# Kernel tuning notes

Hardware: AMD Instinct MI355X
Metric: run time of the kernel (lower is better)

The kernel has to match this reference:

```python
import jax, jax.numpy as jnp
import numpy as np

N = 50000
IN_F = 200
OUT_F = 200
NRELA = 200
E1 = 400000
E2 = 100000
ALPHA = 0.2  # leakyrelu slope


def setup_inputs() -> dict:
    key = jax.random.key(0)
    ks = jax.random.split(key, 9)
    xav = float(np.sqrt(2.0 / (OUT_F + 2 * IN_F + NRELA))) * 1.414
    return {
        "x": jax.random.normal(ks[0], (N, IN_F), dtype=jnp.float32),
        "edge": jax.random.randint(ks[1], (2, E1), 0, N, dtype=jnp.int32),
        "edge_embed": jax.random.normal(ks[2], (E1, NRELA), dtype=jnp.float32),
        "edge_list_nhop": jax.random.randint(ks[3], (2, E2), 0, N, dtype=jnp.int32),
        "edge_embed_nhop": jax.random.normal(ks[4], (E2, NRELA), dtype=jnp.float32),
        "a": jax.random.normal(ks[5], (OUT_F, 2 * IN_F + NRELA), dtype=jnp.float32) * xav,
        "a_2": jax.random.normal(ks[6], (1, OUT_F), dtype=jnp.float32) * float(np.sqrt(2.0 / (1 + OUT_F))) * 1.414,
        "mlp_w": jax.random.normal(ks[7], (1, OUT_F), dtype=jnp.float32) * float(np.sqrt(1.0 / OUT_F)),
        "mlp_b": jnp.zeros((1,), dtype=jnp.float32),
    }


def reference(x, edge, edge_embed, edge_list_nhop, edge_embed_nhop, a, a_2, mlp_w, mlp_b):
    # concat 1-hop and n-hop edges: e [2,E], emb [E,nrela]
    e = jnp.concatenate([edge, edge_list_nhop], axis=1)
    emb = jnp.concatenate([edge_embed, edge_embed_nhop], axis=0)
    src = e[0]
    dst = e[1]
    n_edges = emb.shape[0]
    # edge_h: [E, 2*in + nrela]
    edge_h = jnp.concatenate([x[src], x[dst], emb], axis=1)
    # edge_m = a @ edge_h.T, kept as [E, out]
    edge_m = edge_h @ a.T
    # powers = -leakyrelu(a_2 @ edge_m): [E]
    powers = -jax.nn.leaky_relu(edge_m @ a_2[0], ALPHA)
    # inline MLP: tanh(Linear(edge_m)) -> [E]
    y = jnp.tanh(edge_m @ mlp_w[0] + mlp_b[0])
    powers = powers * y / n_edges
    edge_e = jnp.exp(powers)  # [E]
    n = x.shape[0]
    # segment-sum over source nodes (sparse.sum over dim=1 of coo[src,dst,:])
    e_rowsum = jax.ops.segment_sum(edge_e, src, num_segments=n)[:, None]  # [N,1]
    e_rowsum = jnp.where(e_rowsum == 0.0, 1e-12, e_rowsum)
    # weighted scatter-add of edge messages
    edge_w = edge_e[:, None] * edge_m  # [E, out]
    h_prime = jax.ops.segment_sum(edge_w, src, num_segments=n)  # [N, out]
    h_prime = h_prime / e_rowsum
    return jax.nn.elu(h_prime)  # concat=True
```

## Files before the change

kernel.cpp:

```cpp
#include <hip/hip_runtime.h>
#include <math.h>

#define NN    50000
#define FDIM  200
#define E1N   400000
#define E2N   100000
#define EN    500000

typedef __attribute__((ext_vector_type(8))) short short8;
typedef __attribute__((ext_vector_type(4))) float f32x4;

#define VALL_OFF   0
#define WALL_OFF   608
#define SCAL_OFF   1216
#define RS_OFF     201216
#define CNT_OFF    251216
#define FILL_OFF   301216
#define INCL_OFF   351216
#define BSUM_OFF   401216
#define SORT_OFF   401472
#define XB_OFF     1401472
#define AB_OFF     6401472
#define TSB_OFF    6461472

static __device__ __forceinline__ unsigned short f2bf(float f) {
    unsigned int u = __float_as_uint(f);
    unsigned int r = (u + 0x7fffu + ((u >> 16) & 1u)) >> 16;
    return (unsigned short)r;
}
static __device__ __forceinline__ float bf2f(unsigned short s) {
    return __uint_as_float((unsigned int)s << 16);
}

__global__ void k_coeffs(const float* __restrict__ a, const float* __restrict__ a2,
                         const float* __restrict__ mlpw,
                         float* __restrict__ vall, float* __restrict__ wall) {
    int k = blockIdx.x * blockDim.x + threadIdx.x;
    if (k >= 600) return;
    float v = 0.f, w = 0.f;
    for (int o = 0; o < FDIM; ++o) {
        float av = a[o * 600 + k];
        v += a2[o] * av;
        w += mlpw[o] * av;
    }
    vall[k] = v;
    wall[k] = w;
}

__global__ __launch_bounds__(256) void k_node_scal(const float* __restrict__ x,
                                                   const float* __restrict__ vall,
                                                   const float* __restrict__ wall,
                                                   float* __restrict__ scal,
                                                   unsigned short* __restrict__ xb) {
    __shared__ float sv[1200];
    int tid = threadIdx.x;
    for (int i = tid; i < 1200; i += 256) sv[i] = (i < 600) ? vall[i] : wall[i - 600];
    __syncthreads();
    int lane = tid & 63;
    int n = blockIdx.x * 4 + (tid >> 6);
    float ps = 0.f, pd = 0.f, qs = 0.f, qd = 0.f;
    if (lane < 50) {
        float4 xv = *(const float4*)(x + (size_t)n * FDIM + lane * 4);
        float4 v1 = *(const float4*)(sv + lane * 4);
        float4 v2 = *(const float4*)(sv + 200 + lane * 4);
        float4 w1 = *(const float4*)(sv + 600 + lane * 4);
        float4 w2 = *(const float4*)(sv + 800 + lane * 4);
        ps = xv.x * v1.x + xv.y * v1.y + xv.z * v1.z + xv.w * v1.w;
        pd = xv.x * v2.x + xv.y * v2.y + xv.z * v2.z + xv.w * v2.w;
        qs = xv.x * w1.x + xv.y * w1.y + xv.z * w1.z + xv.w * w1.w;
        qd = xv.x * w2.x + xv.y * w2.y + xv.z * w2.z + xv.w * w2.w;
        ushort4 o;
        o.x = f2bf(xv.x); o.y = f2bf(xv.y); o.z = f2bf(xv.z); o.w = f2bf(xv.w);
        *(ushort4*)(xb + (size_t)n * FDIM + lane * 4) = o;
    }
    #pragma unroll
    for (int off = 32; off > 0; off >>= 1) {
        ps += __shfl_xor(ps, off);
        pd += __shfl_xor(pd, off);
        qs += __shfl_xor(qs, off);
        qd += __shfl_xor(qd, off);
    }
    if (lane == 0) {
        float4 r = make_float4(ps, pd, qs, qd);
        *(float4*)(scal + (size_t)n * 4) = r;
    }
}

__global__ __launch_bounds__(256) void k_cvt(const float* __restrict__ src,
                                             unsigned short* __restrict__ dst, int n4) {
    int i = blockIdx.x * 256 + threadIdx.x;
    if (i >= n4) return;
    float4 v = *(const float4*)(src + (size_t)i * 4);
    ushort4 o;
    o.x = f2bf(v.x); o.y = f2bf(v.y); o.z = f2bf(v.z); o.w = f2bf(v.w);
    *(ushort4*)(dst + (size_t)i * 4) = o;
}

__global__ __launch_bounds__(256) void k_hist(const int* __restrict__ edge,
                                              const int* __restrict__ edgenh,
                                              int* __restrict__ counts) {
    int g = blockIdx.x * 256 + threadIdx.x;
    if (g >= EN) return;
    int s = (g < E1N) ? edge[g] : edgenh[g - E1N];
    atomicAdd(counts + s, 1);
}

__global__ __launch_bounds__(256) void k_scan1(const int* __restrict__ counts,
                                               int* __restrict__ incl,
                                               int* __restrict__ bsums) {
    __shared__ int tmp[256];
    int g = blockIdx.x * 256 + threadIdx.x;
    int v = (g < NN) ? counts[g] : 0;
    tmp[threadIdx.x] = v;
    __syncthreads();
    for (int off = 1; off < 256; off <<= 1) {
        int t = (threadIdx.x >= off) ? tmp[threadIdx.x - off] : 0;
        __syncthreads();
        tmp[threadIdx.x] += t;
        __syncthreads();
    }
    if (g < NN) incl[g] = tmp[threadIdx.x];
    if (threadIdx.x == 255) bsums[blockIdx.x] = tmp[255];
}

__global__ __launch_bounds__(256) void k_scan2(int* __restrict__ bsums, int nb) {
    __shared__ int tmp[256];
    int v = (threadIdx.x < nb) ? bsums[threadIdx.x] : 0;
    tmp[threadIdx.x] = v;
    __syncthreads();
    for (int off = 1; off < 256; off <<= 1) {
        int t = (threadIdx.x >= off) ? tmp[threadIdx.x - off] : 0;
        __syncthreads();
        tmp[threadIdx.x] += t;
        __syncthreads();
    }
    if (threadIdx.x < nb) bsums[threadIdx.x] = tmp[threadIdx.x] - v;
}

__global__ __launch_bounds__(256) void k_scan3(const int* __restrict__ counts,
                                               int* __restrict__ incl,
                                               const int* __restrict__ bsums,
                                               int* __restrict__ fill) {
    int g = blockIdx.x * 256 + threadIdx.x;
    if (g >= NN) return;
    int v = incl[g] - counts[g] + bsums[blockIdx.x];
    incl[g] = v;
    fill[g] = v;
}

__global__ __launch_bounds__(256) void k_scatter(const int* __restrict__ edge,
                                                 const int* __restrict__ edgenh,
                                                 int* __restrict__ fill,
                                                 int2* __restrict__ sorted2) {
    int g = blockIdx.x * 256 + threadIdx.x;
    if (g >= EN) return;
    int s, d;
    if (g < E1N) { s = edge[g]; d = edge[E1N + g]; }
    else { s = edgenh[g - E1N]; d = edgenh[E2N + (g - E1N)]; }
    int pos = atomicAdd(fill + s, 1);
    sorted2[pos] = make_int2(g, d);
}

__global__ __launch_bounds__(256) void k_csr(const int2* __restrict__ sorted2,
                                             const int* __restrict__ offs,
                                             const int* __restrict__ counts,
                                             const float* __restrict__ ee,
                                             const float* __restrict__ eenh,
                                             const unsigned short* __restrict__ xb,
                                             const float* __restrict__ vall,
                                             const float* __restrict__ wall,
                                             const float* __restrict__ scal,
                                             const float* __restrict__ mlpb,
                                             float* __restrict__ rowsum,
                                             unsigned short* __restrict__ Tsb) {
    int tid = threadIdx.x, lane = tid & 63;
    int n = blockIdx.x * 4 + (tid >> 6);
    float4 v3 = make_float4(0, 0, 0, 0), w3 = v3;
    if (lane < 50) {
        v3 = *(const float4*)(vall + 400 + lane * 4);
        w3 = *(const float4*)(wall + 400 + lane * 4);
    }
    float4 sc_n = *(const float4*)(scal + (size_t)n * 4);
    float mb = mlpb[0];
    int beg = offs[n], cnt = counts[n];
    float accx0 = 0, accx1 = 0, accx2 = 0, accx3 = 0;
    float acce0 = 0, acce1 = 0, acce2 = 0, acce3 = 0;
    float rs = 0.f;
    int2 ed = (cnt > 0) ? sorted2[beg] : make_int2(0, 0);
    for (int i = 0; i < cnt; ++i) {
        int2 ed_n = (i + 1 < cnt) ? sorted2[beg + i + 1] : ed;
        int e = ed.x, d = ed.y;
        const float* erow = (e < E1N) ? ee + (size_t)e * FDIM
                                      : eenh + (size_t)(e - E1N) * FDIM;
        float4 ev = make_float4(0, 0, 0, 0), xv = ev;
        if (lane < 50) {
            ev = *(const float4*)(erow + lane * 4);
            ushort4 xu = *(const ushort4*)(xb + (size_t)d * FDIM + lane * 4);
            xv.x = bf2f(xu.x); xv.y = bf2f(xu.y); xv.z = bf2f(xu.z); xv.w = bf2f(xu.w);
        }
        float pe = ev.x * v3.x + ev.y * v3.y + ev.z * v3.z + ev.w * v3.w;
        float qe = ev.x * w3.x + ev.y * w3.y + ev.z * w3.z + ev.w * w3.w;
        #pragma unroll
        for (int off = 32; off > 0; off >>= 1) {
            pe += __shfl_xor(pe, off);
            qe += __shfl_xor(qe, off);
        }
        float4 sd = *(const float4*)(scal + (size_t)d * 4);
        float z1 = sc_n.x + sd.y + pe;
        float z2 = sc_n.z + sd.w + qe + mb;
        float l = z1 > 0.f ? z1 : 0.2f * z1;
        float e2 = __expf(2.f * z2);
        float t = 1.f - 2.f * __builtin_amdgcn_rcpf(e2 + 1.f);
        float wgt = __expf(l * t * (-1.f / (float)EN));
        rs += wgt;
        accx0 += wgt * xv.x; accx1 += wgt * xv.y; accx2 += wgt * xv.z; accx3 += wgt * xv.w;
        acce0 += wgt * ev.x; acce1 += wgt * ev.y; acce2 += wgt * ev.z; acce3 += wgt * ev.w;
        ed = ed_n;
    }
    if (lane == 0) rowsum[n] = rs;
    float inv = (cnt > 0) ? __builtin_amdgcn_rcpf(rs) : 0.f;
    if (lane < 50) {
        ushort4 o1, o2;
        o1.x = f2bf(accx0 * inv); o1.y = f2bf(accx1 * inv);
        o1.z = f2bf(accx2 * inv); o1.w = f2bf(accx3 * inv);
        o2.x = f2bf(acce0 * inv); o2.y = f2bf(acce1 * inv);
        o2.z = f2bf(acce2 * inv); o2.w = f2bf(acce3 * inv);
        *(ushort4*)(Tsb + (size_t)n * 400 + lane * 4) = o1;
        *(ushort4*)(Tsb + (size_t)n * 400 + 200 + lane * 4) = o2;
    }
}

__global__ __launch_bounds__(256) void k_gemm_fused(const unsigned short* __restrict__ xb,
                                                    const unsigned short* __restrict__ tsb,
                                                    const unsigned short* __restrict__ ab,
                                                    const float* __restrict__ rowsum,
                                                    float* __restrict__ out) {
    __shared__ unsigned short Al[64][40];
    __shared__ unsigned short Bl[64][40];
    int tid = threadIdx.x, w = tid >> 6, lane = tid & 63;
    int bx = blockIdx.x, by = blockIdx.y;
    f32x4 acc[4] = {};
    int r = tid >> 2, c = tid & 3;
    int arow = by * 64 + r;
    int brow = bx * 64 + r;
    bool inA = arow < NN;
    bool inB = brow < 200;
    const unsigned short* aPx = xb + (size_t)arow * 200;
    const unsigned short* aPt = tsb + (size_t)arow * 400;
    const unsigned short* bP = ab + (size_t)brow * 600;
    for (int k0 = 0; k0 < 640; k0 += 32) {
        int gk = k0 + c * 8;
        uint4 av = make_uint4(0, 0, 0, 0), bv = av;
        if (gk < 200) {
            if (inA) av = *(const uint4*)(aPx + gk);
            if (inB) bv = *(const uint4*)(bP + gk);
        } else if (gk >= 224 && gk < 624) {
            if (inA) av = *(const uint4*)(aPt + (gk - 224));
            if (inB) bv = *(const uint4*)(bP + gk - 24);
        }
        *(uint4*)&Al[r][c * 8] = av;
        *(uint4*)&Bl[r][c * 8] = bv;
        __syncthreads();
        short8 af = *(short8*)&Al[w * 16 + (lane & 15)][(lane >> 4) * 8];
        #pragma unroll
        for (int ct = 0; ct < 4; ++ct) {
            short8 bf = *(short8*)&Bl[ct * 16 + (lane & 15)][(lane >> 4) * 8];
            acc[ct] = __builtin_amdgcn_mfma_f32_16x16x32_bf16(af, bf, acc[ct], 0, 0, 0);
        }
        __syncthreads();
    }
    #pragma unroll
    for (int ct = 0; ct < 4; ++ct) {
        #pragma unroll
        for (int rr = 0; rr < 4; ++rr) {
            int grow = by * 64 + w * 16 + (lane >> 4) * 4 + rr;
            int gcol = bx * 64 + ct * 16 + (lane & 15);
            if (grow < NN && gcol < 200) {
                float rsv = rowsum[grow];
                float h = acc[ct][rr];
                float o = (rsv == 0.f) ? 0.f : (h > 0.f ? h : expm1f(h));
                out[(size_t)grow * 200 + gcol] = o;
            }
        }
    }
}

extern "C" void kernel_launch(void* const* d_in, const int* in_sizes, int n_in,
                              void* d_out, int out_size, void* d_ws, size_t ws_size,
                              hipStream_t stream) {
    const float* x      = (const float*)d_in[0];
    const int*   edge   = (const int*)d_in[1];
    const float* ee     = (const float*)d_in[2];
    const int*   edgenh = (const int*)d_in[3];
    const float* eenh   = (const float*)d_in[4];
    const float* a      = (const float*)d_in[5];
    const float* a2     = (const float*)d_in[6];
    const float* mlpw   = (const float*)d_in[7];
    const float* mlpb   = (const float*)d_in[8];

    float* ws = (float*)d_ws;
    float* vall   = ws + VALL_OFF;
    float* wall   = ws + WALL_OFF;
    float* scal   = ws + SCAL_OFF;
    float* rowsum = ws + RS_OFF;
    int*   counts = (int*)(ws + CNT_OFF);
    int*   fill   = (int*)(ws + FILL_OFF);
    int*   incl   = (int*)(ws + INCL_OFF);
    int*   bsums  = (int*)(ws + BSUM_OFF);
    int2*  sorted2 = (int2*)(ws + SORT_OFF);
    unsigned short* xb  = (unsigned short*)(ws + XB_OFF);
    unsigned short* ab  = (unsigned short*)(ws + AB_OFF);
    unsigned short* tsb = (unsigned short*)(ws + TSB_OFF);

    hipMemsetAsync(counts, 0, (size_t)(2 * NN) * sizeof(int), stream);

    k_coeffs<<<3, 256, 0, stream>>>(a, a2, mlpw, vall, wall);
    k_node_scal<<<NN / 4, 256, 0, stream>>>(x, vall, wall, scal, xb);
    k_cvt<<<(200 * 600 / 4 + 255) / 256, 256, 0, stream>>>(a, ab, 200 * 600 / 4);

    k_hist<<<(EN + 255) / 256, 256, 0, stream>>>(edge, edgenh, counts);
    int nb = (NN + 255) / 256;
    k_scan1<<<nb, 256, 0, stream>>>(counts, incl, bsums);
    k_scan2<<<1, 256, 0, stream>>>(bsums, nb);
    k_scan3<<<nb, 256, 0, stream>>>(counts, incl, bsums, fill);
    k_scatter<<<(EN + 255) / 256, 256, 0, stream>>>(edge, edgenh, fill, sorted2);

    k_csr<<<NN / 4, 256, 0, stream>>>(sorted2, incl, counts, ee, eenh, xb,
                                      vall, wall, scal, mlpb, rowsum, tsb);

    dim3 gg(4, (NN + 63) / 64);
    k_gemm_fused<<<gg, 256, 0, stream>>>(xb, tsb, ab, rowsum, (float*)d_out);
}
```

Measured before the change: 747.2 us.

## Split edge weight computation into per-edge kernel and remap GEMM block order

Per-edge attention weights are now computed in a separate edge-parallel kernel that writes a weight buffer and accumulates row sums with atomics. The CSR aggregation kernel then only gathers edge embeddings and neighbour features scaled by the precomputed weight, which removes the serial shuffle-reduction and exp chain from its per-node loop. The GEMM block index is also remapped to a swizzled order to change cache locality. The cost is reading every edge embedding twice (once per kernel) plus an extra launch and atomics.

```diff
diff --git a/kernel.cpp b/kernel.cpp
--- a/kernel.cpp
+++ b/kernel.cpp
@@ -22,6 +22,7 @@
 #define XB_OFF     1401472
 #define AB_OFF     6401472
 #define TSB_OFF    6461472
+#define WGT_OFF    16461472
 
 static __device__ __forceinline__ unsigned short f2bf(float f) {
     unsigned int u = __float_as_uint(f);
@@ -161,70 +162,91 @@
     sorted2[pos] = make_int2(g, d);
 }
 
-__global__ __launch_bounds__(256) void k_csr(const int2* __restrict__ sorted2,
-                                             const int* __restrict__ offs,
-                                             const int* __restrict__ counts,
-                                             const float* __restrict__ ee,
-                                             const float* __restrict__ eenh,
-                                             const unsigned short* __restrict__ xb,
-                                             const float* __restrict__ vall,
-                                             const float* __restrict__ wall,
-                                             const float* __restrict__ scal,
-                                             const float* __restrict__ mlpb,
-                                             float* __restrict__ rowsum,
-                                             unsigned short* __restrict__ Tsb) {
+__global__ __launch_bounds__(256) void k_edge_wgt(const int* __restrict__ edge,
+                                                  const int* __restrict__ edgenh,
+                                                  const float* __restrict__ ee,
+                                                  const float* __restrict__ eenh,
+                                                  const float* __restrict__ vall,
+                                                  const float* __restrict__ wall,
+                                                  const float* __restrict__ scal,
+                                                  const float* __restrict__ mlpb,
+                                                  float* __restrict__ wgtbuf,
+                                                  float* __restrict__ rowsum) {
+    int tid = threadIdx.x, lane = tid & 63;
+    int e = blockIdx.x * 4 + (tid >> 6);
+    int s, d;
+    const float* erow;
+    if (e < E1N) {
+        s = edge[e]; d = edge[E1N + e];
+        erow = ee + (size_t)e * FDIM;
+    } else {
+        int f = e - E1N;
+        s = edgenh[f]; d = edgenh[E2N + f];
+        erow = eenh + (size_t)f * FDIM;
+    }
+    float pe = 0.f, qe = 0.f;
+    if (lane < 50) {
+        float4 ev = *(const float4*)(erow + lane * 4);
+        float4 v3 = *(const float4*)(vall + 400 + lane * 4);
+        float4 w3 = *(const float4*)(wall + 400 + lane * 4);
+        pe = ev.x * v3.x + ev.y * v3.y + ev.z * v3.z + ev.w * v3.w;
+        qe = ev.x * w3.x + ev.y * w3.y + ev.z * w3.z + ev.w * w3.w;
+    }
+    #pragma unroll
+    for (int off = 32; off > 0; off >>= 1) {
+        pe += __shfl_xor(pe, off);
+        qe += __shfl_xor(qe, off);
+    }
+    float4 ss = *(const float4*)(scal + (size_t)s * 4);
+    float4 sd = *(const float4*)(scal + (size_t)d * 4);
+    float z1 = ss.x + sd.y + pe;
+    float z2 = ss.z + sd.w + qe + mlpb[0];
+    float l = z1 > 0.f ? z1 : 0.2f * z1;
+    float e2 = __expf(2.f * z2);
+    float t = 1.f - 2.f * __builtin_amdgcn_rcpf(e2 + 1.f);
+    float w = __expf(l * t * (-1.f / (float)EN));
+    if (lane == 0) {
+        wgtbuf[e] = w;
+        atomicAdd(rowsum + s, w);
+    }
+}
+
+__global__ __launch_bounds__(256) void k_csr2(const int2* __restrict__ sorted2,
+                                              const int* __restrict__ offs,
+                                              const int* __restrict__ counts,
+                                              const float* __restrict__ ee,
+                                              const float* __restrict__ eenh,
+                                              const unsigned short* __restrict__ xb,
+                                              const float* __restrict__ wgtbuf,
+                                              const float* __restrict__ rowsum,
+                                              unsigned short* __restrict__ Tsb) {
     int tid = threadIdx.x, lane = tid & 63;
     int n = blockIdx.x * 4 + (tid >> 6);
-    float4 v3 = make_float4(0, 0, 0, 0), w3 = v3;
-    if (lane < 50) {
-        v3 = *(const float4*)(vall + 400 + lane * 4);
-        w3 = *(const float4*)(wall + 400 + lane * 4);
-    }
-    float4 sc_n = *(const float4*)(scal + (size_t)n * 4);
-    float mb = mlpb[0];
     int beg = offs[n], cnt = counts[n];
-    float accx0 = 0, accx1 = 0, accx2 = 0, accx3 = 0;
-    float acce0 = 0, acce1 = 0, acce2 = 0, acce3 = 0;
-    float rs = 0.f;
-    int2 ed = (cnt > 0) ? sorted2[beg] : make_int2(0, 0);
+    float ax0 = 0, ax1 = 0, ax2 = 0, ax3 = 0;
+    float ae0 = 0, ae1 = 0, ae2 = 0, ae3 = 0;
+    #pragma unroll 2
     for (int i = 0; i < cnt; ++i) {
-        int2 ed_n = (i + 1 < cnt) ? sorted2[beg + i + 1] : ed;
-        int e = ed.x, d = ed.y;
-        const float* erow = (e < E1N) ? ee + (size_t)e * FDIM
-                                      : eenh + (size_t)(e - E1N) * FDIM;
+        int2 ed = sorted2[beg + i];
+        float wv = wgtbuf[ed.x];
+        const float* erow = (ed.x < E1N) ? ee + (size_t)ed.x * FDIM
+                                         : eenh + (size_t)(ed.x - E1N) * FDIM;
         float4 ev = make_float4(0, 0, 0, 0), xv = ev;
         if (lane < 50) {
             ev = *(const float4*)(erow + lane * 4);
-            ushort4 xu = *(const ushort4*)(xb + (size_t)d * FDIM + lane * 4);
+            ushort4 xu = *(const ushort4*)(xb + (size_t)ed.y * FDIM + lane * 4);
             xv.x = bf2f(xu.x); xv.y = bf2f(xu.y); xv.z = bf2f(xu.z); xv.w = bf2f(xu.w);
         }
-        float pe = ev.x * v3.x + ev.y * v3.y + ev.z * v3.z + ev.w * v3.w;
-        float qe = ev.x * w3.x + ev.y * w3.y + ev.z * w3.z + ev.w * w3.w;
-        #pragma unroll
-        for (int off = 32; off > 0; off >>= 1) {
-            pe += __shfl_xor(pe, off);
-            qe += __shfl_xor(qe, off);
-        }
-        float4 sd = *(const float4*)(scal + (size_t)d * 4);
-        float z1 = sc_n.x + sd.y + pe;
-        float z2 = sc_n.z + sd.w + qe + mb;
-        float l = z1 > 0.f ? z1 : 0.2f * z1;
-        float e2 = __expf(2.f * z2);
-        float t = 1.f - 2.f * __builtin_amdgcn_rcpf(e2 + 1.f);
-        float wgt = __expf(l * t * (-1.f / (float)EN));
-        rs += wgt;
-        accx0 += wgt * xv.x; accx1 += wgt * xv.y; accx2 += wgt * xv.z; accx3 += wgt * xv.w;
-        acce0 += wgt * ev.x; acce1 += wgt * ev.y; acce2 += wgt * ev.z; acce3 += wgt * ev.w;
-        ed = ed_n;
-    }
-    if (lane == 0) rowsum[n] = rs;
-    float inv = (cnt > 0) ? __builtin_amdgcn_rcpf(rs) : 0.f;
+        ax0 += wv * xv.x; ax1 += wv * xv.y; ax2 += wv * xv.z; ax3 += wv * xv.w;
+        ae0 += wv * ev.x; ae1 += wv * ev.y; ae2 += wv * ev.z; ae3 += wv * ev.w;
+    }
+    float inv = (cnt > 0) ? __builtin_amdgcn_rcpf(rowsum[n]) : 0.f;
     if (lane < 50) {
         ushort4 o1, o2;
-        o1.x = f2bf(accx0 * inv); o1.y = f2bf(accx1 * inv);
-        o1.z = f2bf(accx2 * inv); o1.w = f2bf(accx3 * inv);
-        o2.x = f2bf(acce0 * inv); o2.y = f2bf(acce1 * inv);
-        o2.z = f2bf(acce2 * inv); o2.w = f2bf(acce3 * inv);
+        o1.x = f2bf(ax0 * inv); o1.y = f2bf(ax1 * inv);
+        o1.z = f2bf(ax2 * inv); o1.w = f2bf(ax3 * inv);
+        o2.x = f2bf(ae0 * inv); o2.y = f2bf(ae1 * inv);
+        o2.z = f2bf(ae2 * inv); o2.w = f2bf(ae3 * inv);
         *(ushort4*)(Tsb + (size_t)n * 400 + lane * 4) = o1;
         *(ushort4*)(Tsb + (size_t)n * 400 + 200 + lane * 4) = o2;
     }
@@ -238,7 +260,9 @@
     __shared__ unsigned short Al[64][40];
     __shared__ unsigned short Bl[64][40];
     int tid = threadIdx.x, w = tid >> 6, lane = tid & 63;
-    int bx = blockIdx.x, by = blockIdx.y;
+    int h = blockIdx.y * 4 + blockIdx.x;
+    int g = (h & 7) * 391 + (h >> 3);
+    int by = g >> 2, bx = g & 3;
     f32x4 acc[4] = {};
     int r = tid >> 2, c = tid & 3;
     int arow = by * 64 + r;
@@ -277,8 +301,8 @@
             int gcol = bx * 64 + ct * 16 + (lane & 15);
             if (grow < NN && gcol < 200) {
                 float rsv = rowsum[grow];
-                float h = acc[ct][rr];
-                float o = (rsv == 0.f) ? 0.f : (h > 0.f ? h : expm1f(h));
+                float hh = acc[ct][rr];
+                float o = (rsv == 0.f) ? 0.f : (hh > 0.f ? hh : expm1f(hh));
                 out[(size_t)grow * 200 + gcol] = o;
             }
         }
@@ -311,8 +335,9 @@
     unsigned short* xb  = (unsigned short*)(ws + XB_OFF);
     unsigned short* ab  = (unsigned short*)(ws + AB_OFF);
     unsigned short* tsb = (unsigned short*)(ws + TSB_OFF);
-
-    hipMemsetAsync(counts, 0, (size_t)(2 * NN) * sizeof(int), stream);
+    float* wgtbuf = ws + WGT_OFF;
+
+    hipMemsetAsync(rowsum, 0, (size_t)(3 * NN) * sizeof(int), stream);
 
     k_coeffs<<<3, 256, 0, stream>>>(a, a2, mlpw, vall, wall);
     k_node_scal<<<NN / 4, 256, 0, stream>>>(x, vall, wall, scal, xb);
@@ -325,8 +350,11 @@
     k_scan3<<<nb, 256, 0, stream>>>(counts, incl, bsums, fill);
     k_scatter<<<(EN + 255) / 256, 256, 0, stream>>>(edge, edgenh, fill, sorted2);
 
-    k_csr<<<NN / 4, 256, 0, stream>>>(sorted2, incl, counts, ee, eenh, xb,
-                                      vall, wall, scal, mlpb, rowsum, tsb);
+    k_edge_wgt<<<EN / 4, 256, 0, stream>>>(edge, edgenh, ee, eenh,
+                                           vall, wall, scal, mlpb, wgtbuf, rowsum);
+
+    k_csr2<<<NN / 4, 256, 0, stream>>>(sorted2, incl, counts, ee, eenh, xb,
+                                       wgtbuf, rowsum, tsb);
 
     dim3 gg(4, (NN + 63) / 64);
     k_gemm_fused<<<gg, 256, 0, stream>>>(xb, tsb, ab, rowsum, (float*)d_out);
```

Measured after the change: 857.3 us. 1.15x slower.
